# Optimization experiments

Measured on AMD Instinct MI355X. Metric: run time of the kernel, lower is better.

The kernel has to match this reference:

```python
import jax, jax.numpy as jnp
import numpy as np

N_NODES = 100000
N_EDGES = 1200000
D_IN = 16
D_EDGE = 4
H = 64


def setup_inputs() -> dict:
    key = jax.random.key(0)
    ks = jax.random.split(key, 20)
    s = 0.05
    inp = {
        "src": jax.random.randint(ks[0], (N_EDGES,), 0, N_NODES),
        "dst": jax.random.randint(ks[1], (N_EDGES,), 0, N_NODES),
        "t": jax.random.uniform(ks[2], (N_EDGES,), dtype=jnp.float32),
        "x": jax.random.normal(ks[3], (N_NODES, D_IN), dtype=jnp.float32),
        "edge_attr": jax.random.normal(ks[4], (N_EDGES, D_EDGE), dtype=jnp.float32),
        # x_encoder
        "Wx": jax.random.normal(ks[5], (D_IN, H), dtype=jnp.float32) * s,
        "bx": jnp.zeros((H,), dtype=jnp.float32),
        # TransformerConv (heads=1, concat=False)
        "Wq": jax.random.normal(ks[6], (H, H), dtype=jnp.float32) * s,
        "bq": jnp.zeros((H,), dtype=jnp.float32),
        "Wk": jax.random.normal(ks[7], (H, H), dtype=jnp.float32) * s,
        "bk": jnp.zeros((H,), dtype=jnp.float32),
        "Wv": jax.random.normal(ks[8], (H, H), dtype=jnp.float32) * s,
        "bv": jnp.zeros((H,), dtype=jnp.float32),
        "We": jax.random.normal(ks[9], (D_EDGE, H), dtype=jnp.float32) * s,  # lin_edge, bias=False
        "Ws": jax.random.normal(ks[10], (H, H), dtype=jnp.float32) * s,  # lin_skip (root weight)
        "bs": jnp.zeros((H,), dtype=jnp.float32),
        # MLP head
        "W1": jax.random.normal(ks[11], (H, 8), dtype=jnp.float32) * s,
        "b1": jnp.zeros((8,), dtype=jnp.float32),
        "W2": jax.random.normal(ks[12], (8, 1), dtype=jnp.float32) * s,
        "b2": jnp.zeros((1,), dtype=jnp.float32),
    }
    return inp


def reference(src, dst, t, x, edge_attr, Wx, bx, Wq, bq, Wk, bk, Wv, bv, We, Ws, bs, W1, b1, W2, b2):
    # eval mode: dropouts are identity; TGN memory.update_state is a pure
    # side effect and does not influence the returned output.
    xe = x @ Wx + bx                             # [N, H]

    # TransformerConv, heads=1, concat=False, flow src -> dst
    q = xe @ Wq + bq                             # [N, H]
    k = xe @ Wk + bk                             # [N, H]
    v = xe @ Wv + bv                             # [N, H]
    e = edge_attr @ We                           # [E, H]

    k_e = k[src] + e                             # [E, H]
    v_e = v[src] + e                             # [E, H]
    alpha = jnp.sum(q[dst] * k_e, axis=-1) / jnp.sqrt(jnp.float32(H))  # [E]

    # softmax over incoming edges per destination node
    m = jax.ops.segment_max(alpha, dst, num_segments=N_NODES)
    a = jnp.exp(alpha - m[dst])
    denom = jax.ops.segment_sum(a, dst, num_segments=N_NODES)
    w = a / (denom[dst] + 1e-16)                 # [E]

    agg = jax.ops.segment_sum(v_e * w[:, None], dst, num_segments=N_NODES)  # [N, H]
    h_local = agg + (xe @ Ws + bs)               # root/skip connection

    h = h_local[dst]                             # [E, H]
    h = jax.nn.relu(h @ W1 + b1)                 # [E, 8]
    out = (h @ W2 + b2)[:, 0]                    # [E]
    return out
```

## Files before the change

kernel.cpp:

```cpp
#include <hip/hip_runtime.h>

#define CAP 48

typedef int nint4 __attribute__((ext_vector_type(4)));

#define OFF_M   0
#define OFF_U   256
#define OFF_W   272
#define OFF_C   288
#define OFF_R   292
#define OFF_R0  356
#define OFF_PV  360
#define OFF_PE  488
#define OFF_PS  520
#define OFF_BH1 648
#define OFF_BH2 656
#define CST_N   664

__device__ __forceinline__ unsigned f2bf(float f) {
    unsigned u = __float_as_uint(f);
    u += 0x7fffu + ((u >> 16) & 1u);
    return u >> 16;
}
__device__ __forceinline__ float bf_lo(unsigned u) { return __uint_as_float(u << 16); }
__device__ __forceinline__ float bf_hi(unsigned u) { return __uint_as_float(u & 0xffff0000u); }

struct Params {
    const int* src; const int* dst; const float4* ea4; const float* x;
    const float* Wx; const float* bx;
    const float* Wq; const float* bq;
    const float* Wk; const float* bk;
    const float* Wv; const float* bv;
    const float* We; const float* Ws; const float* bs;
    const float* W1; const float* b1; const float* W2; const float* b2;
    int* cursor; nint4* csr; float* cst;
    float* yv; float* rv; float* cdv; float* g; float* out;
    int N, E;
};

__device__ void do_fold(const Params& P, float* __restrict__ cst)
{
    __shared__ float sWf[4][16][64];
    __shared__ float sbf[4][64];
    const int t = threadIdx.x;
    const int c = t & 63, m = t >> 6;
    const float* W; const float* b;
    switch (m) {
        case 0:  W = P.Wq; b = P.bq; break;
        case 1:  W = P.Wk; b = P.bk; break;
        case 2:  W = P.Wv; b = P.bv; break;
        default: W = P.Ws; b = P.bs; break;
    }
    float acc[16];
#pragma unroll
    for (int i = 0; i < 16; ++i) acc[i] = 0.f;
    float bacc = b[c];
    for (int j = 0; j < 64; ++j) {
        const float wv = W[j * 64 + c];
        bacc += P.bx[j] * wv;
#pragma unroll
        for (int i = 0; i < 16; ++i) acc[i] += P.Wx[i * 64 + j] * wv;
    }
#pragma unroll
    for (int i = 0; i < 16; ++i) sWf[m][i][c] = acc[i];
    sbf[m][c] = bacc;
    __syncthreads();

    {
        const int i = t >> 4, j = t & 15;
        float s = 0.f;
        for (int cc = 0; cc < 64; ++cc) s += sWf[0][i][cc] * sWf[1][j][cc];
        cst[OFF_M + i * 16 + j] = s;
    }
    if (t < 16) {
        float su = 0.f, sw = 0.f;
        for (int cc = 0; cc < 64; ++cc) {
            su += sWf[1][t][cc] * sbf[0][cc];
            sw += sWf[0][t][cc] * sbf[1][cc];
        }
        cst[OFF_U + t] = su;
        cst[OFF_W + t] = sw;
    }
    if (t == 0) {
        float s = 0.f;
        for (int cc = 0; cc < 64; ++cc) s += sbf[0][cc] * sbf[1][cc];
        cst[OFF_C] = s;
    }
    if (t < 64) {
        const int j = t >> 4, i = t & 15;
        float s = 0.f;
        for (int cc = 0; cc < 64; ++cc) s += P.We[j * 64 + cc] * sWf[0][i][cc];
        cst[OFF_R + j * 16 + i] = s;
    }
    if (t < 4) {
        float s = 0.f;
        for (int cc = 0; cc < 64; ++cc) s += P.We[t * 64 + cc] * sbf[0][cc];
        cst[OFF_R0 + t] = s;
    }
    if (t < 128) {
        const int i = t >> 3, j = t & 7;
        float sv = 0.f, ss = 0.f;
        for (int cc = 0; cc < 64; ++cc) {
            const float w1 = P.W1[cc * 8 + j];
            sv += sWf[2][i][cc] * w1;
            ss += sWf[3][i][cc] * w1;
        }
        cst[OFF_PV + i * 8 + j] = sv;
        cst[OFF_PS + i * 8 + j] = ss;
    }
    if (t < 32) {
        const int mm = t >> 3, j = t & 7;
        float s = 0.f;
        for (int cc = 0; cc < 64; ++cc) s += P.We[mm * 64 + cc] * P.W1[cc * 8 + j];
        cst[OFF_PE + mm * 8 + j] = s;
    }
    if (t < 8) {
        float s1 = 0.f, s2 = 0.f;
        for (int cc = 0; cc < 64; ++cc) {
            const float w1 = P.W1[cc * 8 + t];
            s1 += sbf[2][cc] * w1;
            s2 += sbf[3][cc] * w1;
        }
        cst[OFF_BH1 + t] = s1;
        cst[OFF_BH2 + t] = s2 + P.b1[t];
    }
}

__global__ __launch_bounds__(256) void k_init(Params P)
{
    if (blockIdx.x == 0) { do_fold(P, P.cst); return; }
    const int i = (blockIdx.x - 1) * 256 + threadIdx.x;
    if (i < P.N) P.cursor[i] = 0;
}

__global__ __launch_bounds__(256) void k_fill(Params P)
{
    const int t = threadIdx.x;
    const int nbE = (P.E + 255) >> 8;
    if ((int)blockIdx.x < nbE) {
        const int e = blockIdx.x * 256 + t;
        if (e >= P.E) return;
        const int s = P.src[e];
        const int d = P.dst[e];
        const float4 A = P.ea4[e];
        const int pos = atomicAdd(&P.cursor[d], 1);
        if (pos < CAP) {
            nint4 ent;
            ent.x = s;
            ent.y = e;
            ent.z = (int)(f2bf(A.x) | (f2bf(A.y) << 16));
            ent.w = (int)(f2bf(A.z) | (f2bf(A.w) << 16));
            P.csr[(size_t)d * CAP + pos] = ent;
        }
        return;
    }

    __shared__ float sx[16][16];
    const float* __restrict__ cst = P.cst;
    const int node0 = ((int)blockIdx.x - nbE) * 16;
    const int nl = t >> 4, cg = t & 15;
    {
        const int idx = node0 * 16 + t;
        sx[nl][cg] = (idx < P.N * 16) ? P.x[idx] : 0.f;
    }
    __syncthreads();
    const int n = node0 + nl;
    if (n >= P.N) return;

    float y = cst[OFF_U + cg];
#pragma unroll
    for (int i = 0; i < 16; ++i)
        y += sx[nl][i] * cst[OFF_M + i * 16 + cg];
    P.yv[(size_t)n * 16 + cg] = y;

    if (cg < 4) {
        float r = cst[OFF_R0 + cg];
#pragma unroll
        for (int i = 0; i < 16; ++i)
            r += cst[OFF_R + cg * 16 + i] * sx[nl][i];
        P.rv[(size_t)n * 4 + cg] = r;
    } else if (cg == 4) {
        float cd = cst[OFF_C];
#pragma unroll
        for (int i = 0; i < 16; ++i)
            cd += cst[OFF_W + i] * sx[nl][i];
        P.cdv[n] = cd;
    }
}

__global__ __launch_bounds__(128) void k_agg(Params P)
{
    const int t = threadIdx.x;
    const int l = t & 63;
    const int wv = t >> 6;
    const int grp = l >> 4;
    const int cg  = l & 15;
    const int n   = (blockIdx.x * 2 + wv) * 4 + grp;
    const float* __restrict__ cst = P.cst;

    const bool vn = n < P.N;
    const int nn = vn ? n : P.N - 1;
    const int deg = vn ? min(P.cursor[nn], CAP) : 0;
    const size_t nbase = (size_t)nn * CAP;

    const float xd = P.x[(size_t)nn * 16 + cg];
    const float y  = P.yv[(size_t)nn * 16 + cg];
    const float4 rv = *(const float4*)&P.rv[(size_t)nn * 4];
    const float cd = P.cdv[nn];

    int degM = deg;
    degM = max(degM, __shfl_xor(degM, 16));
    degM = max(degM, __shfl_xor(degM, 32));

    float T = 0.f, S0 = 0.f, S1 = 0.f, S2 = 0.f, S3 = 0.f, den = 0.f;

    for (int i = 0; i < degM; i += 2) {
        const bool va = i < deg;
        const bool vb = (i + 1) < deg;
        const nint4 Ea = P.csr[nbase + (va ? i : 0)];
        const nint4 Eb = P.csr[nbase + (vb ? i + 1 : 0)];
        const int sa = va ? Ea.x : 0;
        const int sb = vb ? Eb.x : 0;
        const float xsa = P.x[(size_t)sa * 16 + cg];
        const float xsb = P.x[(size_t)sb * 16 + cg];
        {
            const float A0 = bf_lo((unsigned)Ea.z), A1 = bf_hi((unsigned)Ea.z);
            const float A2 = bf_lo((unsigned)Ea.w), A3 = bf_hi((unsigned)Ea.w);
            float p = y * xsa;
            p += __shfl_xor(p, 1);
            p += __shfl_xor(p, 2);
            p += __shfl_xor(p, 4);
            p += __shfl_xor(p, 8);
            p += cd + A0 * rv.x + A1 * rv.y + A2 * rv.z + A3 * rv.w;
            const float a = va ? __expf(p * 0.125f) : 0.f;
            T += a * xsa;
            S0 += a * A0; S1 += a * A1; S2 += a * A2; S3 += a * A3;
            den += a;
        }
        {
            const float A0 = bf_lo((unsigned)Eb.z), A1 = bf_hi((unsigned)Eb.z);
            const float A2 = bf_lo((unsigned)Eb.w), A3 = bf_hi((unsigned)Eb.w);
            float p = y * xsb;
            p += __shfl_xor(p, 1);
            p += __shfl_xor(p, 2);
            p += __shfl_xor(p, 4);
            p += __shfl_xor(p, 8);
            p += cd + A0 * rv.x + A1 * rv.y + A2 * rv.z + A3 * rv.w;
            const float a = vb ? __expf(p * 0.125f) : 0.f;
            T += a * xsb;
            S0 += a * A0; S1 += a * A1; S2 += a * A2; S3 += a * A3;
            den += a;
        }
    }

    const float inv = 1.f / (den + 1e-16f);
    const float Ti = T * inv;

    float hp[8];
#pragma unroll
    for (int j = 0; j < 8; ++j)
        hp[j] = Ti * cst[OFF_PV + cg * 8 + j] + xd * cst[OFF_PS + cg * 8 + j];
#pragma unroll
    for (int j = 0; j < 8; ++j) {
        hp[j] += __shfl_xor(hp[j], 1);
        hp[j] += __shfl_xor(hp[j], 2);
        hp[j] += __shfl_xor(hp[j], 4);
        hp[j] += __shfl_xor(hp[j], 8);
    }
    const float dinv = den * inv;
    float val = P.b2[0];
#pragma unroll
    for (int j = 0; j < 8; ++j) {
        const float hid = hp[j]
            + inv * (S0 * cst[OFF_PE + 0 * 8 + j] + S1 * cst[OFF_PE + 1 * 8 + j]
                   + S2 * cst[OFF_PE + 2 * 8 + j] + S3 * cst[OFF_PE + 3 * 8 + j])
            + dinv * cst[OFF_BH1 + j] + cst[OFF_BH2 + j];
        val += fmaxf(hid, 0.f) * P.W2[j];
    }

    if (cg == 0 && vn) P.g[n] = val;
}

__global__ __launch_bounds__(256) void k_out(
    const int* __restrict__ dst, const float* __restrict__ g,
    float* __restrict__ out, int E)
{
    const int e = blockIdx.x * 256 + threadIdx.x;
    if (e < E) out[e] = g[dst[e]];
}

extern "C" void kernel_launch(void* const* d_in, const int* in_sizes, int n_in,
                              void* d_out, int out_size, void* d_ws, size_t ws_size,
                              hipStream_t stream)
{
    Params P;
    P.src = (const int*)d_in[0];
    P.dst = (const int*)d_in[1];
    P.x   = (const float*)d_in[3];
    P.ea4 = (const float4*)d_in[4];
    P.Wx  = (const float*)d_in[5];
    P.bx  = (const float*)d_in[6];
    P.Wq  = (const float*)d_in[7];
    P.bq  = (const float*)d_in[8];
    P.Wk  = (const float*)d_in[9];
    P.bk  = (const float*)d_in[10];
    P.Wv  = (const float*)d_in[11];
    P.bv  = (const float*)d_in[12];
    P.We  = (const float*)d_in[13];
    P.Ws  = (const float*)d_in[14];
    P.bs  = (const float*)d_in[15];
    P.W1  = (const float*)d_in[16];
    P.b1  = (const float*)d_in[17];
    P.W2  = (const float*)d_in[18];
    P.b2  = (const float*)d_in[19];

    P.E = in_sizes[0];
    P.N = in_sizes[3] / 16;
    P.out = (float*)d_out;

    P.csr    = (nint4*)d_ws;
    P.cursor = (int*)(P.csr + (size_t)P.N * CAP);
    P.cst    = (float*)(P.cursor + P.N);
    P.yv     = P.cst + CST_N;
    P.rv     = P.yv + (size_t)P.N * 16;
    P.cdv    = P.rv + (size_t)P.N * 4;
    P.g      = P.cdv + P.N;

    const int nbE = (P.E + 255) / 256;
    const int nbN16 = (P.N + 15) / 16;

    k_init<<<1 + (P.N + 255) / 256, 256, 0, stream>>>(P);
    k_fill<<<nbE + nbN16, 256, 0, stream>>>(P);
    k_agg<<<(P.N + 7) / 8, 128, 0, stream>>>(P);
    k_out<<<nbE, 256, 0, stream>>>(P.dst, P.g, P.out, P.E);
}
```

Before: 252.6 us.

## Replace CSR bucketing with edge-parallel atomic scatter of projected messages

Drops the per-destination CSR build and the per-node gather loop. Each edge now computes its attention logit and scatters the exponentiated weight times a pre-projected 8-wide message (value and edge terms already pushed through W1) into per-node accumulators with float atomics. A separate per-node kernel then normalises and applies the MLP head. This avoids the CAP-sized bucket writes and degree-imbalanced loops, and the per-destination constant term is dropped because it cancels in the softmax. The cost is about nine float atomics per edge to random addresses, plus nondeterministic accumulation order.

```diff
diff --git a/kernel.cpp b/kernel.cpp
--- a/kernel.cpp
+++ b/kernel.cpp
@@ -1,8 +1,4 @@
 #include <hip/hip_runtime.h>
-
-#define CAP 48
-
-typedef int nint4 __attribute__((ext_vector_type(4)));
 
 #define OFF_M   0
 #define OFF_U   256
@@ -17,14 +13,6 @@
 #define OFF_BH2 656
 #define CST_N   664
 
-__device__ __forceinline__ unsigned f2bf(float f) {
-    unsigned u = __float_as_uint(f);
-    u += 0x7fffu + ((u >> 16) & 1u);
-    return u >> 16;
-}
-__device__ __forceinline__ float bf_lo(unsigned u) { return __uint_as_float(u << 16); }
-__device__ __forceinline__ float bf_hi(unsigned u) { return __uint_as_float(u & 0xffff0000u); }
-
 struct Params {
     const int* src; const int* dst; const float4* ea4; const float* x;
     const float* Wx; const float* bx;
@@ -33,8 +21,15 @@
     const float* Wv; const float* bv;
     const float* We; const float* Ws; const float* bs;
     const float* W1; const float* b1; const float* W2; const float* b2;
-    int* cursor; nint4* csr; float* cst;
-    float* yv; float* rv; float* cdv; float* g; float* out;
+    float* cst;
+    float* yv;
+    float* pv;
+    float* xps;
+    float* H;
+    float4* rv4;
+    float* den;
+    float* g;
+    float* out;
     int N, E;
 };
 
@@ -128,36 +123,15 @@
 
 __global__ __launch_bounds__(256) void k_init(Params P)
 {
-    if (blockIdx.x == 0) { do_fold(P, P.cst); return; }
-    const int i = (blockIdx.x - 1) * 256 + threadIdx.x;
-    if (i < P.N) P.cursor[i] = 0;
-}
-
-__global__ __launch_bounds__(256) void k_fill(Params P)
-{
-    const int t = threadIdx.x;
-    const int nbE = (P.E + 255) >> 8;
-    if ((int)blockIdx.x < nbE) {
-        const int e = blockIdx.x * 256 + t;
-        if (e >= P.E) return;
-        const int s = P.src[e];
-        const int d = P.dst[e];
-        const float4 A = P.ea4[e];
-        const int pos = atomicAdd(&P.cursor[d], 1);
-        if (pos < CAP) {
-            nint4 ent;
-            ent.x = s;
-            ent.y = e;
-            ent.z = (int)(f2bf(A.x) | (f2bf(A.y) << 16));
-            ent.w = (int)(f2bf(A.z) | (f2bf(A.w) << 16));
-            P.csr[(size_t)d * CAP + pos] = ent;
-        }
-        return;
-    }
-
+    do_fold(P, P.cst);
+}
+
+__global__ __launch_bounds__(256) void k_node(Params P)
+{
     __shared__ float sx[16][16];
     const float* __restrict__ cst = P.cst;
-    const int node0 = ((int)blockIdx.x - nbE) * 16;
+    const int t = threadIdx.x;
+    const int node0 = blockIdx.x * 16;
     const int nl = t >> 4, cg = t & 15;
     {
         const int idx = node0 * 16 + t;
@@ -173,112 +147,84 @@
         y += sx[nl][i] * cst[OFF_M + i * 16 + cg];
     P.yv[(size_t)n * 16 + cg] = y;
 
+    if (cg < 8) {
+        float s = 0.f;
+#pragma unroll
+        for (int i = 0; i < 16; ++i)
+            s += sx[nl][i] * cst[OFF_PV + i * 8 + cg];
+        P.pv[(size_t)n * 8 + cg] = s;
+        P.H[(size_t)n * 8 + cg] = 0.f;
+    } else {
+        const int j = cg - 8;
+        float s = 0.f;
+#pragma unroll
+        for (int i = 0; i < 16; ++i)
+            s += sx[nl][i] * cst[OFF_PS + i * 8 + j];
+        P.xps[(size_t)n * 8 + j] = s;
+    }
     if (cg < 4) {
         float r = cst[OFF_R0 + cg];
 #pragma unroll
         for (int i = 0; i < 16; ++i)
             r += cst[OFF_R + cg * 16 + i] * sx[nl][i];
-        P.rv[(size_t)n * 4 + cg] = r;
+        ((float*)P.rv4)[(size_t)n * 4 + cg] = r;
     } else if (cg == 4) {
-        float cd = cst[OFF_C];
-#pragma unroll
-        for (int i = 0; i < 16; ++i)
-            cd += cst[OFF_W + i] * sx[nl][i];
-        P.cdv[n] = cd;
-    }
-}
-
-__global__ __launch_bounds__(128) void k_agg(Params P)
+        P.den[n] = 0.f;
+    }
+}
+
+__global__ __launch_bounds__(256) void k_edge(Params P)
 {
     const int t = threadIdx.x;
-    const int l = t & 63;
-    const int wv = t >> 6;
-    const int grp = l >> 4;
-    const int cg  = l & 15;
-    const int n   = (blockIdx.x * 2 + wv) * 4 + grp;
+    const int grp = t >> 3;
+    const int cg  = t & 7;
+    const int e = blockIdx.x * 32 + grp;
+    const bool ve = e < P.E;
+    const int ee = ve ? e : 0;
+
+    const int s = P.src[ee];
+    const int d = P.dst[ee];
+    const float4 A = P.ea4[ee];
+    const float2 xs2 = ((const float2*)P.x)[(size_t)s * 8 + cg];
+    const float2 yd2 = ((const float2*)P.yv)[(size_t)d * 8 + cg];
+    const float4 rv = P.rv4[d];
+
+    float p = xs2.x * yd2.x + xs2.y * yd2.y;
+    p += __shfl_xor(p, 1);
+    p += __shfl_xor(p, 2);
+    p += __shfl_xor(p, 4);
+    p += A.x * rv.x + A.y * rv.y + A.z * rv.z + A.w * rv.w;
+    const float a = __expf(p * 0.125f);
+
+    if (ve) {
+        const float* __restrict__ cst = P.cst;
+        const float pe = A.x * cst[OFF_PE + 0 * 8 + cg]
+                       + A.y * cst[OFF_PE + 1 * 8 + cg]
+                       + A.z * cst[OFF_PE + 2 * 8 + cg]
+                       + A.w * cst[OFF_PE + 3 * 8 + cg];
+        const float pvs = P.pv[(size_t)s * 8 + cg];
+        atomicAdd(&P.H[(size_t)d * 8 + cg], a * (pvs + pe));
+        if (cg == 0) atomicAdd(&P.den[d], a);
+    }
+}
+
+__global__ __launch_bounds__(256) void k_fin(Params P)
+{
+    const int n = blockIdx.x * 256 + threadIdx.x;
+    if (n >= P.N) return;
     const float* __restrict__ cst = P.cst;
-
-    const bool vn = n < P.N;
-    const int nn = vn ? n : P.N - 1;
-    const int deg = vn ? min(P.cursor[nn], CAP) : 0;
-    const size_t nbase = (size_t)nn * CAP;
-
-    const float xd = P.x[(size_t)nn * 16 + cg];
-    const float y  = P.yv[(size_t)nn * 16 + cg];
-    const float4 rv = *(const float4*)&P.rv[(size_t)nn * 4];
-    const float cd = P.cdv[nn];
-
-    int degM = deg;
-    degM = max(degM, __shfl_xor(degM, 16));
-    degM = max(degM, __shfl_xor(degM, 32));
-
-    float T = 0.f, S0 = 0.f, S1 = 0.f, S2 = 0.f, S3 = 0.f, den = 0.f;
-
-    for (int i = 0; i < degM; i += 2) {
-        const bool va = i < deg;
-        const bool vb = (i + 1) < deg;
-        const nint4 Ea = P.csr[nbase + (va ? i : 0)];
-        const nint4 Eb = P.csr[nbase + (vb ? i + 1 : 0)];
-        const int sa = va ? Ea.x : 0;
-        const int sb = vb ? Eb.x : 0;
-        const float xsa = P.x[(size_t)sa * 16 + cg];
-        const float xsb = P.x[(size_t)sb * 16 + cg];
-        {
-            const float A0 = bf_lo((unsigned)Ea.z), A1 = bf_hi((unsigned)Ea.z);
-            const float A2 = bf_lo((unsigned)Ea.w), A3 = bf_hi((unsigned)Ea.w);
-            float p = y * xsa;
-            p += __shfl_xor(p, 1);
-            p += __shfl_xor(p, 2);
-            p += __shfl_xor(p, 4);
-            p += __shfl_xor(p, 8);
-            p += cd + A0 * rv.x + A1 * rv.y + A2 * rv.z + A3 * rv.w;
-            const float a = va ? __expf(p * 0.125f) : 0.f;
-            T += a * xsa;
-            S0 += a * A0; S1 += a * A1; S2 += a * A2; S3 += a * A3;
-            den += a;
-        }
-        {
-            const float A0 = bf_lo((unsigned)Eb.z), A1 = bf_hi((unsigned)Eb.z);
-            const float A2 = bf_lo((unsigned)Eb.w), A3 = bf_hi((unsigned)Eb.w);
-            float p = y * xsb;
-            p += __shfl_xor(p, 1);
-            p += __shfl_xor(p, 2);
-            p += __shfl_xor(p, 4);
-            p += __shfl_xor(p, 8);
-            p += cd + A0 * rv.x + A1 * rv.y + A2 * rv.z + A3 * rv.w;
-            const float a = vb ? __expf(p * 0.125f) : 0.f;
-            T += a * xsb;
-            S0 += a * A0; S1 += a * A1; S2 += a * A2; S3 += a * A3;
-            den += a;
-        }
-    }
-
+    const float den = P.den[n];
     const float inv = 1.f / (den + 1e-16f);
-    const float Ti = T * inv;
-
-    float hp[8];
-#pragma unroll
-    for (int j = 0; j < 8; ++j)
-        hp[j] = Ti * cst[OFF_PV + cg * 8 + j] + xd * cst[OFF_PS + cg * 8 + j];
-#pragma unroll
-    for (int j = 0; j < 8; ++j) {
-        hp[j] += __shfl_xor(hp[j], 1);
-        hp[j] += __shfl_xor(hp[j], 2);
-        hp[j] += __shfl_xor(hp[j], 4);
-        hp[j] += __shfl_xor(hp[j], 8);
-    }
     const float dinv = den * inv;
     float val = P.b2[0];
 #pragma unroll
     for (int j = 0; j < 8; ++j) {
-        const float hid = hp[j]
-            + inv * (S0 * cst[OFF_PE + 0 * 8 + j] + S1 * cst[OFF_PE + 1 * 8 + j]
-                   + S2 * cst[OFF_PE + 2 * 8 + j] + S3 * cst[OFF_PE + 3 * 8 + j])
-            + dinv * cst[OFF_BH1 + j] + cst[OFF_BH2 + j];
+        const float hid = inv * P.H[(size_t)n * 8 + j]
+                        + P.xps[(size_t)n * 8 + j]
+                        + dinv * cst[OFF_BH1 + j] + cst[OFF_BH2 + j];
         val += fmaxf(hid, 0.f) * P.W2[j];
     }
-
-    if (cg == 0 && vn) P.g[n] = val;
+    P.g[n] = val;
 }
 
 __global__ __launch_bounds__(256) void k_out(
@@ -318,19 +264,21 @@
     P.N = in_sizes[3] / 16;
     P.out = (float*)d_out;
 
-    P.csr    = (nint4*)d_ws;
-    P.cursor = (int*)(P.csr + (size_t)P.N * CAP);
-    P.cst    = (float*)(P.cursor + P.N);
-    P.yv     = P.cst + CST_N;
-    P.rv     = P.yv + (size_t)P.N * 16;
-    P.cdv    = P.rv + (size_t)P.N * 4;
-    P.g      = P.cdv + P.N;
+    float* w = (float*)d_ws;
+    P.yv  = w;            w += (size_t)P.N * 16;
+    P.pv  = w;            w += (size_t)P.N * 8;
+    P.xps = w;            w += (size_t)P.N * 8;
+    P.H   = w;            w += (size_t)P.N * 8;
+    P.rv4 = (float4*)w;   w += (size_t)P.N * 4;
+    P.den = w;            w += (size_t)P.N;
+    P.g   = w;            w += (size_t)P.N;
+    P.cst = w;
 
     const int nbE = (P.E + 255) / 256;
-    const int nbN16 = (P.N + 15) / 16;
-
-    k_init<<<1 + (P.N + 255) / 256, 256, 0, stream>>>(P);
-    k_fill<<<nbE + nbN16, 256, 0, stream>>>(P);
-    k_agg<<<(P.N + 7) / 8, 128, 0, stream>>>(P);
+
+    k_init<<<1, 256, 0, stream>>>(P);
+    k_node<<<(P.N + 15) / 16, 256, 0, stream>>>(P);
+    k_edge<<<(P.E + 31) / 32, 256, 0, stream>>>(P);
+    k_fin<<<(P.N + 255) / 256, 256, 0, stream>>>(P);
     k_out<<<nbE, 256, 0, stream>>>(P.dst, P.g, P.out, P.E);
 }
```

Result: slower. 283.1 us (+12.1%).
